# Kernel optimization log

Measured on AMD Instinct MI355X. Metric: run time of the kernel, lower is better.

Reference implementation:

```python
import jax, jax.numpy as jnp
import numpy as np

N_NODES = 16384
N_EDGES = 262144
DIM = 256
N_BLOCKS = 200


def setup_inputs() -> dict:
    key = jax.random.key(0)
    k1, k2, k3, k4, k5 = jax.random.split(key, 5)
    x = jax.random.normal(k1, (N_NODES, DIM), dtype=jnp.float32)
    W = jax.random.normal(k2, (DIM, DIM), dtype=jnp.float32) * 0.05
    b = jax.random.normal(k3, (DIM,), dtype=jnp.float32) * 0.05
    edge_index = jax.random.randint(k4, (2, N_EDGES), 0, N_NODES, dtype=jnp.int64)
    sec_ids = jax.random.randint(k5, (N_NODES,), 0, N_BLOCKS, dtype=jnp.int64)
    return {"x": x, "W": W, "b": b, "edge_index": edge_index, "sec_ids": sec_ids}


def reference(x, W, b, edge_index, sec_ids):
    # ResidueIntraBlockGNN: keep only intra-block edges, then GCNConv.
    # Filtering is expressed as edge_weight in {0,1} (mathematically identical
    # to dropping the edges, since gcn_norm weights degrees and messages by it).
    N = x.shape[0]
    row, col = edge_index[0], edge_index[1]
    ew = (sec_ids[row] == sec_ids[col]).astype(x.dtype)  # [E] intra-block mask

    # GCNConv default: add self-loops with weight 1
    loop = jnp.arange(N)
    src = jnp.concatenate([row, loop])          # [E+N] message sources
    dst = jnp.concatenate([col, loop])          # [E+N] message targets
    w = jnp.concatenate([ew, jnp.ones((N,), dtype=x.dtype)])

    # symmetric normalization: deg over targets, norm = d^-1/2[src]*w*d^-1/2[dst]
    deg = jax.ops.segment_sum(w, dst, num_segments=N)
    dinv = jnp.where(deg > 0, jax.lax.rsqrt(jnp.maximum(deg, 1e-12)), 0.0)
    norm = dinv[src] * w * dinv[dst]            # [E+N]

    h = x @ W                                   # [N, dim] linear (bias after agg)
    msg = h[src] * norm[:, None]                # gather + scale
    out = jax.ops.segment_sum(msg, dst, num_segments=N)  # scatter-add
    return out + b
```

## Files before the change

kernel.cpp:

```cpp
#include <hip/hip_runtime.h>
#include <hip/hip_bf16.h>

#define N_NODES 16384
#define N_EDGES 262144
#define DIM 256

typedef __attribute__((ext_vector_type(4))) float f32x4;
typedef __attribute__((ext_vector_type(8))) short bf16x8;

__device__ inline short f2bf(float f) {
    union { float f; unsigned u; } v; v.f = f;
    unsigned r = v.u + 0x7fffu + ((v.u >> 16) & 1u);
    return (short)(r >> 16);
}


__global__ void k_prep(const float* __restrict__ W, short* __restrict__ Wt,
                       unsigned* __restrict__ deg, unsigned* __restrict__ count) {
    int bid = blockIdx.x;
    int tid = threadIdx.x;
    if (bid < 256) {
        int idx = bid * 256 + tid;
        int n = idx >> 8, k = idx & 255;
        Wt[idx] = f2bf(W[k * 256 + n]);
    } else {
        int i = (bid - 256) * 256 + tid;
        deg[i] = 1u;
        if (i == 0) *count = 0u;
    }
}

__global__ void k_edges(const int* __restrict__ ei, const int* __restrict__ sec,
                        unsigned* __restrict__ deg, unsigned* __restrict__ count,
                        int2* __restrict__ list) {
    int e = blockIdx.x * blockDim.x + threadIdx.x;
    if (e >= N_EDGES) return;
    int r = ei[e];
    int c = ei[N_EDGES + e];
    if (sec[r] == sec[c]) {
        atomicAdd(&deg[c], 1u);
        unsigned pos = atomicAdd(count, 1u);
        list[pos] = make_int2(r, c);
    }
}

__global__ __launch_bounds__(256) void k_gemm(
        const float* __restrict__ x, const short* __restrict__ Wt,
        const float* __restrict__ b, const unsigned* __restrict__ deg,
        float* __restrict__ h, float* __restrict__ out) {
    const int lane = threadIdx.x & 63;
    const int wave = threadIdx.x >> 6;
    const int r16  = lane & 15;
    const int kg   = lane >> 4;
    const int bm   = blockIdx.x * 64 + wave * 16;

    const float* xrow = x + (size_t)(bm + r16) * DIM + kg * 8;

    f32x4 xa[8][2];
    #pragma unroll
    for (int ks = 0; ks < 8; ++ks) {
        xa[ks][0] = *reinterpret_cast<const f32x4*>(xrow + ks * 32);
        xa[ks][1] = *reinterpret_cast<const f32x4*>(xrow + ks * 32 + 4);
    }

    f32x4 acc[16];
    #pragma unroll
    for (int i = 0; i < 16; ++i) acc[i] = (f32x4)0.f;

    const short* wp = Wt + (size_t)r16 * DIM + kg * 8;

    #pragma unroll
    for (int ks = 0; ks < 8; ++ks) {
        bf16x8 a;
        #pragma unroll
        for (int j = 0; j < 4; ++j) {
            a[j]     = f2bf(xa[ks][0][j]);
            a[4 + j] = f2bf(xa[ks][1][j]);
        }
        #pragma unroll
        for (int nf = 0; nf < 16; ++nf) {
            bf16x8 bv = *reinterpret_cast<const bf16x8*>(wp + (size_t)nf * 16 * DIM + ks * 32);
            acc[nf] = __builtin_amdgcn_mfma_f32_16x16x32_bf16(a, bv, acc[nf], 0, 0, 0);
        }
    }

    const int rbase = bm + kg * 4;
    uint4 dv = *reinterpret_cast<const uint4*>(deg + rbase);
    float inv[4] = {1.f / (float)dv.x, 1.f / (float)dv.y,
                    1.f / (float)dv.z, 1.f / (float)dv.w};
    #pragma unroll
    for (int nf = 0; nf < 16; ++nf) {
        int n = nf * 16 + r16;
        float bn = b[n];
        #pragma unroll
        for (int r = 0; r < 4; ++r) {
            float hv = acc[nf][r];
            h[(size_t)(rbase + r) * DIM + n]   = hv;
            out[(size_t)(rbase + r) * DIM + n] = hv * inv[r] + bn;
        }
    }
}

__global__ void k_scatter(const float* __restrict__ h, const unsigned* __restrict__ deg,
                          const unsigned* __restrict__ count, const int2* __restrict__ list,
                          float* __restrict__ out) {
    unsigned nact = *count;
    unsigned wv     = (blockIdx.x * blockDim.x + threadIdx.x) >> 6;
    unsigned lane   = threadIdx.x & 63;
    unsigned nwaves = (gridDim.x * blockDim.x) >> 6;
    for (unsigned e = wv; e < nact; e += nwaves) {
        int2 rc = list[e];
        float norm = rsqrtf((float)deg[rc.x]) * rsqrtf((float)deg[rc.y]);
        float4 hv = *reinterpret_cast<const float4*>(&h[(size_t)rc.x * DIM + lane * 4]);
        float* o = &out[(size_t)rc.y * DIM + lane * 4];
        atomicAdd(o + 0, hv.x * norm);
        atomicAdd(o + 1, hv.y * norm);
        atomicAdd(o + 2, hv.z * norm);
        atomicAdd(o + 3, hv.w * norm);
    }
}

extern "C" void kernel_launch(void* const* d_in, const int* in_sizes, int n_in,
                              void* d_out, int out_size, void* d_ws, size_t ws_size,
                              hipStream_t stream) {
    const float* x  = (const float*)d_in[0];
    const float* W  = (const float*)d_in[1];
    const float* b  = (const float*)d_in[2];
    const int* ei   = (const int*)d_in[3];
    const int* sec  = (const int*)d_in[4];
    float* out      = (float*)d_out;

    char* ws = (char*)d_ws;
    unsigned* deg   = (unsigned*)ws;
    unsigned* count = (unsigned*)(ws + 65536);
    int2* list      = (int2*)(ws + 65536 + 256);
    size_t wt_off = 65536 + 256 + (size_t)N_EDGES * sizeof(int2);
    wt_off = (wt_off + 255) & ~(size_t)255;
    short* Wt = (short*)(ws + wt_off);
    size_t h_off = wt_off + (size_t)DIM * DIM * sizeof(short);
    h_off = (h_off + 255) & ~(size_t)255;
    float* h = (float*)(ws + h_off);

    k_prep<<<320, 256, 0, stream>>>(W, Wt, deg, count);
    k_edges<<<N_EDGES / 256, 256, 0, stream>>>(ei, sec, deg, count, list);
    k_gemm<<<N_NODES / 64, 256, 0, stream>>>(x, Wt, b, deg, h, out);
    k_scatter<<<256, 256, 0, stream>>>(h, deg, count, list, out);
}
```

Before: 54.70 us.

## Fuse all four stages into one cooperative kernel with grid syncs

Replaces the four separate launches (prep, edge filter, GEMM, scatter) with one cooperative kernel of 256 blocks that uses grid.sync between phases, removing per-launch overhead and gaps between kernels. It also adds a per-node source flag so h rows are written only for nodes that act as sources of intra-block edges, which cuts h write traffic. The GEMM x loads are now software-pipelined one k-step ahead instead of all preloaded. In exchange, the code depends on cooperative launch with all blocks co-resident, and each grid sync adds a global barrier.

```diff
diff --git a/kernel.cpp b/kernel.cpp
--- a/kernel.cpp
+++ b/kernel.cpp
@@ -1,9 +1,13 @@
 #include <hip/hip_runtime.h>
-#include <hip/hip_bf16.h>
+#include <hip/hip_cooperative_groups.h>
+
+namespace cg = cooperative_groups;
 
 #define N_NODES 16384
 #define N_EDGES 262144
 #define DIM 256
+#define NBLK 256
+#define NTHR 256
 
 typedef __attribute__((ext_vector_type(4))) float f32x4;
 typedef __attribute__((ext_vector_type(8))) short bf16x8;
@@ -15,108 +19,109 @@
 }
 
 
-__global__ void k_prep(const float* __restrict__ W, short* __restrict__ Wt,
-                       unsigned* __restrict__ deg, unsigned* __restrict__ count) {
-    int bid = blockIdx.x;
-    int tid = threadIdx.x;
-    if (bid < 256) {
-        int idx = bid * 256 + tid;
-        int n = idx >> 8, k = idx & 255;
-        Wt[idx] = f2bf(W[k * 256 + n]);
-    } else {
-        int i = (bid - 256) * 256 + tid;
-        deg[i] = 1u;
-        if (i == 0) *count = 0u;
+__global__ __launch_bounds__(256, 1) void k_fused(
+        const float* __restrict__ x, const float* __restrict__ W,
+        const float* __restrict__ b, const int* __restrict__ ei,
+        const int* __restrict__ sec,
+        unsigned* deg, unsigned* count, unsigned char* srcflag,
+        int2* list, short* Wt, float* h, float* out) {
+    cg::grid_group grid = cg::this_grid();
+    const int tid = threadIdx.x;
+    const int g = blockIdx.x * NTHR + tid;
+
+    {
+        int n = g >> 8, k = g & 255;
+        Wt[g] = f2bf(W[k * 256 + n]);
+        if (g < N_NODES) { deg[g] = 1u; srcflag[g] = 0; }
+        if (g == 0) *count = 0u;
     }
-}
-
-__global__ void k_edges(const int* __restrict__ ei, const int* __restrict__ sec,
-                        unsigned* __restrict__ deg, unsigned* __restrict__ count,
-                        int2* __restrict__ list) {
-    int e = blockIdx.x * blockDim.x + threadIdx.x;
-    if (e >= N_EDGES) return;
-    int r = ei[e];
-    int c = ei[N_EDGES + e];
-    if (sec[r] == sec[c]) {
-        atomicAdd(&deg[c], 1u);
-        unsigned pos = atomicAdd(count, 1u);
-        list[pos] = make_int2(r, c);
-    }
-}
-
-__global__ __launch_bounds__(256) void k_gemm(
-        const float* __restrict__ x, const short* __restrict__ Wt,
-        const float* __restrict__ b, const unsigned* __restrict__ deg,
-        float* __restrict__ h, float* __restrict__ out) {
-    const int lane = threadIdx.x & 63;
-    const int wave = threadIdx.x >> 6;
-    const int r16  = lane & 15;
-    const int kg   = lane >> 4;
-    const int bm   = blockIdx.x * 64 + wave * 16;
-
-    const float* xrow = x + (size_t)(bm + r16) * DIM + kg * 8;
-
-    f32x4 xa[8][2];
-    #pragma unroll
-    for (int ks = 0; ks < 8; ++ks) {
-        xa[ks][0] = *reinterpret_cast<const f32x4*>(xrow + ks * 32);
-        xa[ks][1] = *reinterpret_cast<const f32x4*>(xrow + ks * 32 + 4);
-    }
-
-    f32x4 acc[16];
-    #pragma unroll
-    for (int i = 0; i < 16; ++i) acc[i] = (f32x4)0.f;
-
-    const short* wp = Wt + (size_t)r16 * DIM + kg * 8;
+    grid.sync();
 
     #pragma unroll
-    for (int ks = 0; ks < 8; ++ks) {
-        bf16x8 a;
+    for (int it = 0; it < N_EDGES / (NBLK * NTHR); ++it) {
+        int e = g + it * NBLK * NTHR;
+        int r = ei[e];
+        int c = ei[N_EDGES + e];
+        if (sec[r] == sec[c]) {
+            atomicAdd(&deg[c], 1u);
+            srcflag[r] = 1;
+            unsigned pos = atomicAdd(count, 1u);
+            list[pos] = make_int2(r, c);
+        }
+    }
+    grid.sync();
+
+    {
+        const int lane = tid & 63;
+        const int wave = tid >> 6;
+        const int r16  = lane & 15;
+        const int kg   = lane >> 4;
+        const int bm   = blockIdx.x * 64 + wave * 16;
+
+        const float* xrow = x + (size_t)(bm + r16) * DIM + kg * 8;
+        const short* wp   = Wt + r16 * DIM + kg * 8;
+
+        f32x4 acc[16];
         #pragma unroll
-        for (int j = 0; j < 4; ++j) {
-            a[j]     = f2bf(xa[ks][0][j]);
-            a[4 + j] = f2bf(xa[ks][1][j]);
+        for (int i = 0; i < 16; ++i) acc[i] = (f32x4)0.f;
+
+        f32x4 nx0 = *reinterpret_cast<const f32x4*>(xrow);
+        f32x4 nx1 = *reinterpret_cast<const f32x4*>(xrow + 4);
+        #pragma unroll
+        for (int ks = 0; ks < 8; ++ks) {
+            f32x4 c0 = nx0, c1 = nx1;
+            if (ks < 7) {
+                nx0 = *reinterpret_cast<const f32x4*>(xrow + (ks + 1) * 32);
+                nx1 = *reinterpret_cast<const f32x4*>(xrow + (ks + 1) * 32 + 4);
+            }
+            bf16x8 a;
+            #pragma unroll
+            for (int j = 0; j < 4; ++j) { a[j] = f2bf(c0[j]); a[4 + j] = f2bf(c1[j]); }
+            #pragma unroll
+            for (int nf = 0; nf < 16; ++nf) {
+                bf16x8 bv = *reinterpret_cast<const bf16x8*>(wp + nf * 16 * DIM + ks * 32);
+                acc[nf] = __builtin_amdgcn_mfma_f32_16x16x32_bf16(a, bv, acc[nf], 0, 0, 0);
+            }
+        }
+
+        const int rbase = bm + kg * 4;
+        uint4 dv = *reinterpret_cast<const uint4*>(deg + rbase);
+        unsigned sf4 = *reinterpret_cast<const unsigned*>(srcflag + rbase);
+        float inv[4] = {1.f / (float)dv.x, 1.f / (float)dv.y,
+                        1.f / (float)dv.z, 1.f / (float)dv.w};
+        #pragma unroll
+        for (int nf = 0; nf < 16; ++nf) {
+            int n = nf * 16 + r16;
+            float bn = b[n];
+            #pragma unroll
+            for (int r = 0; r < 4; ++r)
+                out[(size_t)(rbase + r) * DIM + n] = acc[nf][r] * inv[r] + bn;
         }
         #pragma unroll
-        for (int nf = 0; nf < 16; ++nf) {
-            bf16x8 bv = *reinterpret_cast<const bf16x8*>(wp + (size_t)nf * 16 * DIM + ks * 32);
-            acc[nf] = __builtin_amdgcn_mfma_f32_16x16x32_bf16(a, bv, acc[nf], 0, 0, 0);
+        for (int r = 0; r < 4; ++r) {
+            if ((sf4 >> (8 * r)) & 1) {
+                #pragma unroll
+                for (int nf = 0; nf < 16; ++nf)
+                    h[(size_t)(rbase + r) * DIM + nf * 16 + r16] = acc[nf][r];
+            }
         }
     }
+    grid.sync();
 
-    const int rbase = bm + kg * 4;
-    uint4 dv = *reinterpret_cast<const uint4*>(deg + rbase);
-    float inv[4] = {1.f / (float)dv.x, 1.f / (float)dv.y,
-                    1.f / (float)dv.z, 1.f / (float)dv.w};
-    #pragma unroll
-    for (int nf = 0; nf < 16; ++nf) {
-        int n = nf * 16 + r16;
-        float bn = b[n];
-        #pragma unroll
-        for (int r = 0; r < 4; ++r) {
-            float hv = acc[nf][r];
-            h[(size_t)(rbase + r) * DIM + n]   = hv;
-            out[(size_t)(rbase + r) * DIM + n] = hv * inv[r] + bn;
+    {
+        unsigned nact = *count;
+        unsigned wv   = g >> 6;
+        unsigned lane = tid & 63;
+        for (unsigned e = wv; e < nact; e += (NBLK * NTHR) / 64) {
+            int2 rc = list[e];
+            float norm = rsqrtf((float)deg[rc.x]) * rsqrtf((float)deg[rc.y]);
+            f32x4 hv = *reinterpret_cast<const f32x4*>(&h[(size_t)rc.x * DIM + lane * 4]);
+            float* o = &out[(size_t)rc.y * DIM + lane * 4];
+            atomicAdd(o + 0, hv[0] * norm);
+            atomicAdd(o + 1, hv[1] * norm);
+            atomicAdd(o + 2, hv[2] * norm);
+            atomicAdd(o + 3, hv[3] * norm);
         }
-    }
-}
-
-__global__ void k_scatter(const float* __restrict__ h, const unsigned* __restrict__ deg,
-                          const unsigned* __restrict__ count, const int2* __restrict__ list,
-                          float* __restrict__ out) {
-    unsigned nact = *count;
-    unsigned wv     = (blockIdx.x * blockDim.x + threadIdx.x) >> 6;
-    unsigned lane   = threadIdx.x & 63;
-    unsigned nwaves = (gridDim.x * blockDim.x) >> 6;
-    for (unsigned e = wv; e < nact; e += nwaves) {
-        int2 rc = list[e];
-        float norm = rsqrtf((float)deg[rc.x]) * rsqrtf((float)deg[rc.y]);
-        float4 hv = *reinterpret_cast<const float4*>(&h[(size_t)rc.x * DIM + lane * 4]);
-        float* o = &out[(size_t)rc.y * DIM + lane * 4];
-        atomicAdd(o + 0, hv.x * norm);
-        atomicAdd(o + 1, hv.y * norm);
-        atomicAdd(o + 2, hv.z * norm);
-        atomicAdd(o + 3, hv.w * norm);
     }
 }
 
@@ -131,18 +136,16 @@
     float* out      = (float*)d_out;
 
     char* ws = (char*)d_ws;
-    unsigned* deg   = (unsigned*)ws;
-    unsigned* count = (unsigned*)(ws + 65536);
-    int2* list      = (int2*)(ws + 65536 + 256);
-    size_t wt_off = 65536 + 256 + (size_t)N_EDGES * sizeof(int2);
-    wt_off = (wt_off + 255) & ~(size_t)255;
-    short* Wt = (short*)(ws + wt_off);
-    size_t h_off = wt_off + (size_t)DIM * DIM * sizeof(short);
-    h_off = (h_off + 255) & ~(size_t)255;
-    float* h = (float*)(ws + h_off);
+    unsigned* deg        = (unsigned*)ws;
+    unsigned* count      = (unsigned*)(ws + 65536);
+    unsigned char* sflag = (unsigned char*)(ws + 65792);
+    int2* list           = (int2*)(ws + 82176);
+    short* Wt            = (short*)(ws + 2179328);
+    float* h             = (float*)(ws + 2310400);
 
-    k_prep<<<320, 256, 0, stream>>>(W, Wt, deg, count);
-    k_edges<<<N_EDGES / 256, 256, 0, stream>>>(ei, sec, deg, count, list);
-    k_gemm<<<N_NODES / 64, 256, 0, stream>>>(x, Wt, b, deg, h, out);
-    k_scatter<<<256, 256, 0, stream>>>(h, deg, count, list, out);
+    void* args[] = {(void*)&x, (void*)&W, (void*)&b, (void*)&ei, (void*)&sec,
+                    (void*)&deg, (void*)&count, (void*)&sflag, (void*)&list,
+                    (void*)&Wt, (void*)&h, (void*)&out};
+    hipLaunchCooperativeKernel((const void*)k_fused, dim3(NBLK), dim3(NTHR),
+                               args, 0, stream);
 }
```

Result: slower. 137.1 us (+150.6%).

## Split GEMM into column tiles, XCD-aware block mapping, skip h stores for unused sources

Applied to the files above, without the earlier changes.

The GEMM grid is split into 64x64 output tiles with 1024 blocks instead of 256 full-row blocks. Blocks are mapped so that each XCD handles a contiguous range of rows. X loads are now software-prefetched one k-step ahead rather than all held in registers. A per-node source flag set in the edge kernel lets the GEMM write h only for rows that are sources of intra-block edges, cutting h write traffic. Each x row is now read and converted by four blocks instead of one, and the edge kernel gains an extra byte store per edge.

```diff
diff --git a/kernel.cpp b/kernel.cpp
--- a/kernel.cpp
+++ b/kernel.cpp
@@ -1,5 +1,4 @@
 #include <hip/hip_runtime.h>
-#include <hip/hip_bf16.h>
 
 #define N_NODES 16384
 #define N_EDGES 262144
@@ -16,7 +15,8 @@
 
 
 __global__ void k_prep(const float* __restrict__ W, short* __restrict__ Wt,
-                       unsigned* __restrict__ deg, unsigned* __restrict__ count) {
+                       unsigned* __restrict__ deg, unsigned char* __restrict__ srcflag,
+                       unsigned* __restrict__ count) {
     int bid = blockIdx.x;
     int tid = threadIdx.x;
     if (bid < 256) {
@@ -26,19 +26,21 @@
     } else {
         int i = (bid - 256) * 256 + tid;
         deg[i] = 1u;
+        srcflag[i] = 0;
         if (i == 0) *count = 0u;
     }
 }
 
 __global__ void k_edges(const int* __restrict__ ei, const int* __restrict__ sec,
-                        unsigned* __restrict__ deg, unsigned* __restrict__ count,
-                        int2* __restrict__ list) {
+                        unsigned* __restrict__ deg, unsigned char* __restrict__ srcflag,
+                        unsigned* __restrict__ count, int2* __restrict__ list) {
     int e = blockIdx.x * blockDim.x + threadIdx.x;
     if (e >= N_EDGES) return;
     int r = ei[e];
     int c = ei[N_EDGES + e];
     if (sec[r] == sec[c]) {
         atomicAdd(&deg[c], 1u);
+        srcflag[r] = 1;
         unsigned pos = atomicAdd(count, 1u);
         list[pos] = make_int2(r, c);
     }
@@ -47,56 +49,67 @@
 __global__ __launch_bounds__(256) void k_gemm(
         const float* __restrict__ x, const short* __restrict__ Wt,
         const float* __restrict__ b, const unsigned* __restrict__ deg,
+        const unsigned char* __restrict__ srcflag,
         float* __restrict__ h, float* __restrict__ out) {
-    const int lane = threadIdx.x & 63;
-    const int wave = threadIdx.x >> 6;
+    const int L   = blockIdx.x;
+    const int xcd = L & 7;
+    const int li  = L >> 3;
+    const int rb  = xcd * 32 + (li >> 2);
+    const int cb  = li & 3;
+
+    const int tid  = threadIdx.x;
+    const int lane = tid & 63;
+    const int wave = tid >> 6;
     const int r16  = lane & 15;
     const int kg   = lane >> 4;
-    const int bm   = blockIdx.x * 64 + wave * 16;
+    const int bm   = rb * 64 + wave * 16;
+    const int bn   = cb * 64;
 
     const float* xrow = x + (size_t)(bm + r16) * DIM + kg * 8;
+    const short* wp   = Wt + (size_t)(bn + r16) * DIM + kg * 8;
 
-    f32x4 xa[8][2];
+    f32x4 acc[4];
+    #pragma unroll
+    for (int i = 0; i < 4; ++i) acc[i] = (f32x4)0.f;
+
+    f32x4 nx0 = *reinterpret_cast<const f32x4*>(xrow);
+    f32x4 nx1 = *reinterpret_cast<const f32x4*>(xrow + 4);
     #pragma unroll
     for (int ks = 0; ks < 8; ++ks) {
-        xa[ks][0] = *reinterpret_cast<const f32x4*>(xrow + ks * 32);
-        xa[ks][1] = *reinterpret_cast<const f32x4*>(xrow + ks * 32 + 4);
-    }
-
-    f32x4 acc[16];
-    #pragma unroll
-    for (int i = 0; i < 16; ++i) acc[i] = (f32x4)0.f;
-
-    const short* wp = Wt + (size_t)r16 * DIM + kg * 8;
-
-    #pragma unroll
-    for (int ks = 0; ks < 8; ++ks) {
+        f32x4 c0 = nx0, c1 = nx1;
+        if (ks < 7) {
+            nx0 = *reinterpret_cast<const f32x4*>(xrow + (ks + 1) * 32);
+            nx1 = *reinterpret_cast<const f32x4*>(xrow + (ks + 1) * 32 + 4);
+        }
         bf16x8 a;
         #pragma unroll
-        for (int j = 0; j < 4; ++j) {
-            a[j]     = f2bf(xa[ks][0][j]);
-            a[4 + j] = f2bf(xa[ks][1][j]);
-        }
+        for (int j = 0; j < 4; ++j) { a[j] = f2bf(c0[j]); a[4 + j] = f2bf(c1[j]); }
         #pragma unroll
-        for (int nf = 0; nf < 16; ++nf) {
-            bf16x8 bv = *reinterpret_cast<const bf16x8*>(wp + (size_t)nf * 16 * DIM + ks * 32);
+        for (int nf = 0; nf < 4; ++nf) {
+            bf16x8 bv = *reinterpret_cast<const bf16x8*>(wp + nf * 16 * DIM + ks * 32);
             acc[nf] = __builtin_amdgcn_mfma_f32_16x16x32_bf16(a, bv, acc[nf], 0, 0, 0);
         }
     }
 
     const int rbase = bm + kg * 4;
     uint4 dv = *reinterpret_cast<const uint4*>(deg + rbase);
+    unsigned sf4 = *reinterpret_cast<const unsigned*>(srcflag + rbase);
     float inv[4] = {1.f / (float)dv.x, 1.f / (float)dv.y,
                     1.f / (float)dv.z, 1.f / (float)dv.w};
     #pragma unroll
-    for (int nf = 0; nf < 16; ++nf) {
-        int n = nf * 16 + r16;
-        float bn = b[n];
+    for (int nf = 0; nf < 4; ++nf) {
+        int n = bn + nf * 16 + r16;
+        float bn_ = b[n];
         #pragma unroll
-        for (int r = 0; r < 4; ++r) {
-            float hv = acc[nf][r];
-            h[(size_t)(rbase + r) * DIM + n]   = hv;
-            out[(size_t)(rbase + r) * DIM + n] = hv * inv[r] + bn;
+        for (int r = 0; r < 4; ++r)
+            out[(size_t)(rbase + r) * DIM + n] = acc[nf][r] * inv[r] + bn_;
+    }
+    #pragma unroll
+    for (int r = 0; r < 4; ++r) {
+        if ((sf4 >> (8 * r)) & 1) {
+            #pragma unroll
+            for (int nf = 0; nf < 4; ++nf)
+                h[(size_t)(rbase + r) * DIM + bn + nf * 16 + r16] = acc[nf][r];
         }
     }
 }
@@ -111,12 +124,12 @@
     for (unsigned e = wv; e < nact; e += nwaves) {
         int2 rc = list[e];
         float norm = rsqrtf((float)deg[rc.x]) * rsqrtf((float)deg[rc.y]);
-        float4 hv = *reinterpret_cast<const float4*>(&h[(size_t)rc.x * DIM + lane * 4]);
+        f32x4 hv = *reinterpret_cast<const f32x4*>(&h[(size_t)rc.x * DIM + lane * 4]);
         float* o = &out[(size_t)rc.y * DIM + lane * 4];
-        atomicAdd(o + 0, hv.x * norm);
-        atomicAdd(o + 1, hv.y * norm);
-        atomicAdd(o + 2, hv.z * norm);
-        atomicAdd(o + 3, hv.w * norm);
+        atomicAdd(o + 0, hv[0] * norm);
+        atomicAdd(o + 1, hv[1] * norm);
+        atomicAdd(o + 2, hv[2] * norm);
+        atomicAdd(o + 3, hv[3] * norm);
     }
 }
 
@@ -131,18 +144,15 @@
     float* out      = (float*)d_out;
 
     char* ws = (char*)d_ws;
-    unsigned* deg   = (unsigned*)ws;
-    unsigned* count = (unsigned*)(ws + 65536);
-    int2* list      = (int2*)(ws + 65536 + 256);
-    size_t wt_off = 65536 + 256 + (size_t)N_EDGES * sizeof(int2);
-    wt_off = (wt_off + 255) & ~(size_t)255;
-    short* Wt = (short*)(ws + wt_off);
-    size_t h_off = wt_off + (size_t)DIM * DIM * sizeof(short);
-    h_off = (h_off + 255) & ~(size_t)255;
-    float* h = (float*)(ws + h_off);
+    unsigned* deg        = (unsigned*)ws;
+    unsigned* count      = (unsigned*)(ws + 65536);
+    unsigned char* sflag = (unsigned char*)(ws + 65792);
+    int2* list           = (int2*)(ws + 82176);
+    short* Wt            = (short*)(ws + 2179328);
+    float* h             = (float*)(ws + 2310400);
 
-    k_prep<<<320, 256, 0, stream>>>(W, Wt, deg, count);
-    k_edges<<<N_EDGES / 256, 256, 0, stream>>>(ei, sec, deg, count, list);
-    k_gemm<<<N_NODES / 64, 256, 0, stream>>>(x, Wt, b, deg, h, out);
+    k_prep<<<320, 256, 0, stream>>>(W, Wt, deg, sflag, count);
+    k_edges<<<N_EDGES / 256, 256, 0, stream>>>(ei, sec, deg, sflag, count, list);
+    k_gemm<<<1024, 256, 0, stream>>>(x, Wt, b, deg, sflag, h, out);
     k_scatter<<<256, 256, 0, stream>>>(h, deg, count, list, out);
 }
```

Result: slower. 58.53 us (+7.0%).
